# Performance work log

Measured on AMD Instinct MI355X. Metric: run time of the kernel, lower is better.

Reference implementation:

```python
import jax, jax.numpy as jnp
import numpy as np

NUM_BANDS = 8
WINDOW = 2048
OVERLAP = 1024
SR = 16000


def _band_mask(L):
    # Replicates torch: band = searchsorted(band_ranges, |freq|, left) - 1.
    # DC bin gives band=-1 which torch negative-indexes into the LAST band,
    # hence the mod. All bins satisfy band < NUM_BANDS, so all are assigned.
    freqs = np.fft.fftfreq(L, 1.0 / SR)
    ranges = np.linspace(0.0, SR / 2.0, NUM_BANDS + 1)
    idx = np.searchsorted(ranges, np.abs(freqs), side='left') - 1
    idx = idx % NUM_BANDS
    mask = (idx[None, :] == np.arange(NUM_BANDS)[:, None]).astype(np.float32)
    return jnp.asarray(mask)  # [bands, L]


def _band_signals(x):
    # mag*exp(i*phase) of masked bins == masked complex bins; ifft().real per band
    L = x.shape[-1]
    X = jnp.fft.fft(x)                         # [B, L] complex
    mask = _band_mask(L)                       # [bands, L]
    Xb = X[:, None, :] * mask[None, :, :]      # [B, bands, L]
    return jnp.fft.ifft(Xb).real               # [B, bands, L]


def _chunks(sig):
    L = sig.shape[-1]
    hop = WINDOW - OVERLAP
    n = (L - OVERLAP) // hop                   # num_chunks (static)
    idx = (jnp.arange(n) * hop)[:, None] + jnp.arange(WINDOW)[None, :]  # [n, W]
    return sig[:, :, idx]                       # [B, bands, n, W]


def _loudness(x):
    # BS.1770-style energy loudness (vectorized stand-in for the repo's
    # undefined `loudness` helper): -0.691 + 10*log10(mean square)
    ms = jnp.mean(x * x, axis=-1)
    return -0.691 + 10.0 * jnp.log10(ms + 1e-12)


def reference(watermarked_signals, original_signals):
    ro = _band_signals(original_signals)
    rw = _band_signals(watermarked_signals)
    lo = _loudness(_chunks(ro))                # [B, bands, n]
    lw = _loudness(_chunks(rw))
    lo = jnp.where(jnp.isnan(lo), 0.0, lo)
    lw = jnp.where(jnp.isnan(lw), 0.0, lw)
    diff = (lw - lo).reshape(-1)               # ordered (i, j, k) like the torch loop
    w = jax.nn.softmax(diff)
    return jnp.sum(w * diff)


def setup_inputs() -> dict:
    key = jax.random.key(0)
    k1, k2 = jax.random.split(key)
    B, L = 8, 160000
    return {
        'watermarked_signals': jax.random.normal(k1, (B, L), dtype=jnp.float32),
        'original_signals': jax.random.normal(k2, (B, L), dtype=jnp.float32),
    }
```

## Files before the change

### kernel.cpp

```cpp
#include <hip/hip_runtime.h>
#include <math.h>

constexpr int L      = 160000;
constexpr int BATCH  = 8;
constexpr int NB     = 8;
constexpr int NHOPS  = 156;
constexpr int NCHUNK = 155;
constexpr float TWO_PI = 6.28318530717958647692f;

__device__ __forceinline__ float2 cmulf(float2 a, float2 b) {
  return make_float2(a.x * b.x - a.y * b.y, a.x * b.y + a.y * b.x);
}

template <int SIGN>
__device__ __forceinline__ void bf4s(float2* v) {
  float2 t0 = make_float2(v[0].x + v[2].x, v[0].y + v[2].y);
  float2 t1 = make_float2(v[0].x - v[2].x, v[0].y - v[2].y);
  float2 t2 = make_float2(v[1].x + v[3].x, v[1].y + v[3].y);
  float2 t3 = make_float2(v[1].x - v[3].x, v[1].y - v[3].y);
  v[0] = make_float2(t0.x + t2.x, t0.y + t2.y);
  v[2] = make_float2(t0.x - t2.x, t0.y - t2.y);
  if constexpr (SIGN < 0) {
    v[1] = make_float2(t1.x + t3.y, t1.y - t3.x);
    v[3] = make_float2(t1.x - t3.y, t1.y + t3.x);
  } else {
    v[1] = make_float2(t1.x - t3.y, t1.y + t3.x);
    v[3] = make_float2(t1.x + t3.y, t1.y - t3.x);
  }
}

template <int SIGN>
__device__ __forceinline__ void bf5s(float2* v) {
  const float c1 = 0.30901699437494745f, s1 = 0.9510565162951535f;
  const float c2 = -0.8090169943749475f, s2 = 0.5877852522924731f;
  float2 t1 = make_float2(v[1].x + v[4].x, v[1].y + v[4].y);
  float2 t3 = make_float2(v[1].x - v[4].x, v[1].y - v[4].y);
  float2 t2 = make_float2(v[2].x + v[3].x, v[2].y + v[3].y);
  float2 t4 = make_float2(v[2].x - v[3].x, v[2].y - v[3].y);
  float2 a = make_float2(v[0].x + c1 * t1.x + c2 * t2.x, v[0].y + c1 * t1.y + c2 * t2.y);
  float2 b = make_float2(s1 * t3.x + s2 * t4.x, s1 * t3.y + s2 * t4.y);
  float2 c = make_float2(v[0].x + c2 * t1.x + c1 * t2.x, v[0].y + c2 * t1.y + c1 * t2.y);
  float2 d = make_float2(s2 * t3.x - s1 * t4.x, s2 * t3.y - s1 * t4.y);
  v[0] = make_float2(v[0].x + t1.x + t2.x, v[0].y + t1.y + t2.y);
  if constexpr (SIGN < 0) {
    v[1] = make_float2(a.x + b.y, a.y - b.x);
    v[4] = make_float2(a.x - b.y, a.y + b.x);
    v[2] = make_float2(c.x + d.y, c.y - d.x);
    v[3] = make_float2(c.x - d.y, c.y + d.x);
  } else {
    v[1] = make_float2(a.x - b.y, a.y + b.x);
    v[4] = make_float2(a.x + b.y, a.y - b.x);
    v[2] = make_float2(c.x - d.y, c.y + d.x);
    v[3] = make_float2(c.x + d.y, c.y - d.x);
  }
}

template <int R>
__device__ __forceinline__ void twapply(float2* v, float ang) {
#pragma unroll
  for (int r = 1; r < R; ++r) {
    float s, c;
    __sincosf(ang * (float)r, &s, &c);
    v[r] = cmulf(v[r], make_float2(c, s));
  }
}

__device__ __forceinline__ int rev3_5(int q) {
  int q5 = q / 5, q25 = q / 25;
  int d0 = q - 5 * q5, d1 = q5 - 5 * q25;
  return 25 * d0 + 5 * d1 + q25;
}

__device__ __forceinline__ int rev3_4(int q) {
  return ((q & 3) << 4) | (q & 12) | (q >> 4);
}

template <int SUB, int SIGN>
__device__ __forceinline__ void dif5_ip_stage(float2* a, int ln) {
  int i1 = ln, i2 = ln + 64;
  bool g2 = (i2 < 125);
  int j1 = i1 % SUB, j2 = i2 % SUB;
  int b1 = (i1 / SUB) * (5 * SUB) + j1;
  int b2 = (i2 / SUB) * (5 * SUB) + j2;
  float2 u[5], v[5];
#pragma unroll
  for (int r = 0; r < 5; ++r) u[r] = a[b1 + SUB * r];
  if (g2) {
#pragma unroll
    for (int r = 0; r < 5; ++r) v[r] = a[b2 + SUB * r];
  }
  bf5s<SIGN>(u);
  twapply<5>(u, (float)SIGN * (TWO_PI / (float)(5 * SUB)) * (float)j1);
  if (g2) {
    bf5s<SIGN>(v);
    twapply<5>(v, (float)SIGN * (TWO_PI / (float)(5 * SUB)) * (float)j2);
  }
#pragma unroll
  for (int r = 0; r < 5; ++r) a[b1 + SUB * r] = u[r];
  if (g2) {
#pragma unroll
    for (int r = 0; r < 5; ++r) a[b2 + SUB * r] = v[r];
  }
}

template <int SIGN>
__device__ __forceinline__ void dif625_ip(float2* a, int ln) {
  dif5_ip_stage<125, SIGN>(a, ln);
  dif5_ip_stage<25, SIGN>(a, ln);
  dif5_ip_stage<5, SIGN>(a, ln);
  int q1 = ln, q2 = ln + 64;
  bool g2 = (q2 < 125);
  float2 u[5], v[5];
#pragma unroll
  for (int r = 0; r < 5; ++r) u[r] = a[5 * q1 + r];
  if (g2) {
#pragma unroll
    for (int r = 0; r < 5; ++r) v[r] = a[5 * q2 + r];
  }
  bf5s<SIGN>(u);
  if (g2) bf5s<SIGN>(v);
  int rv1 = rev3_5(q1), rv2 = rev3_5(q2);
#pragma unroll
  for (int r = 0; r < 5; ++r) a[125 * r + rv1] = u[r];
  if (g2) {
#pragma unroll
    for (int r = 0; r < 5; ++r) a[125 * r + rv2] = v[r];
  }
}

template <int SIGN>
__device__ __forceinline__ void dif256_ip(float2* a, int ln) {
  {
    float2 u[4];
#pragma unroll
    for (int r = 0; r < 4; ++r) u[r] = a[ln + 64 * r];
    bf4s<SIGN>(u);
    twapply<4>(u, (float)SIGN * (TWO_PI / 256.0f) * (float)ln);
#pragma unroll
    for (int r = 0; r < 4; ++r) a[ln + 64 * r] = u[r];
  }
  {
    int j = ln & 15, b = 64 * (ln >> 4) + j;
    float2 u[4];
#pragma unroll
    for (int r = 0; r < 4; ++r) u[r] = a[b + 16 * r];
    bf4s<SIGN>(u);
    twapply<4>(u, (float)SIGN * (TWO_PI / 64.0f) * (float)j);
#pragma unroll
    for (int r = 0; r < 4; ++r) a[b + 16 * r] = u[r];
  }
  {
    int j = ln & 3, b = 16 * (ln >> 2) + j;
    float2 u[4];
#pragma unroll
    for (int r = 0; r < 4; ++r) u[r] = a[b + 4 * r];
    bf4s<SIGN>(u);
    twapply<4>(u, (float)SIGN * (TWO_PI / 16.0f) * (float)j);
#pragma unroll
    for (int r = 0; r < 4; ++r) a[b + 4 * r] = u[r];
  }
  {
    float2 u[4];
#pragma unroll
    for (int r = 0; r < 4; ++r) u[r] = a[4 * ln + r];
    bf4s<SIGN>(u);
    int rv = rev3_4(ln);
#pragma unroll
    for (int r = 0; r < 4; ++r) a[64 * r + rv] = u[r];
  }
}

__global__ __launch_bounds__(256) void f1_kernel(const float* __restrict__ win,
                                                 const float* __restrict__ oin,
                                                 float2* __restrict__ G) {
  __shared__ float2 A[4 * 625];
  int blk = blockIdx.x;
  int sig = blk >> 6, g = blk & 63;
  int n1base = g * 4;
  int tid = threadIdx.x;
  const float4* wp4 = (const float4*)(win + (size_t)sig * L);
  const float4* op4 = (const float4*)(oin + (size_t)sig * L);
  for (int r = tid; r < 625; r += 256) {
    float4 wv = wp4[r * 64 + g];
    float4 ov = op4[r * 64 + g];
    A[0 * 625 + r] = make_float2(wv.x, ov.x);
    A[1 * 625 + r] = make_float2(wv.y, ov.y);
    A[2 * 625 + r] = make_float2(wv.z, ov.z);
    A[3 * 625 + r] = make_float2(wv.w, ov.w);
  }
  __syncthreads();
  int wv_ = tid >> 6, ln = tid & 63;
  dif625_ip<-1>(A + wv_ * 625, ln);
  __syncthreads();
  for (int idx = tid; idx < 2500; idx += 256) {
    int k2 = idx >> 2, cc = idx & 3;
    int n1 = n1base + cc;
    float ang = -(TWO_PI / (float)L) * (float)(n1 * k2);
    float s, c;
    __sincosf(ang, &s, &c);
    G[(size_t)sig * L + k2 * 256 + n1] = cmulf(A[cc * 625 + k2], make_float2(c, s));
  }
}

__global__ __launch_bounds__(256) void f2_kernel(const float2* __restrict__ G,
                                                 float2* __restrict__ X) {
  __shared__ float2 A[4 * 257];
  int blk = blockIdx.x;
  int sig = blk / 157, gr = blk % 157;
  int k2base = gr * 4;
  int tid = threadIdx.x;
  int wv = tid >> 6, ln = tid & 63;
  int k2 = k2base + wv;
  float2* a = A + wv * 257;
  if (k2 < 625) {
#pragma unroll
    for (int r = 0; r < 4; ++r) a[ln + 64 * r] = G[(size_t)sig * L + k2 * 256 + ln + 64 * r];
    dif256_ip<-1>(a, ln);
  }
  __syncthreads();
  for (int idx = tid; idx < 1024; idx += 256) {
    int row = idx >> 8, k1 = idx & 255;
    int k2e = k2base + row;
    if (k2e < 625) X[(size_t)sig * L + k2e * 256 + k1] = A[row * 257 + k1];
  }
}

__global__ __launch_bounds__(256) void i1_kernel(const float2* __restrict__ X,
                                                 float2* __restrict__ H) {
  __shared__ float2 A[16 * 257];
  int blk = blockIdx.x;
  int gr = blk % 40, sb = blk / 40;
  int band = sb & 7, sig = sb >> 3;
  int k2base = gr * 16;
  int tid = threadIdx.x;
  int wv = tid >> 6, ln = tid & 63;
  int lo1, hi1, lo2, hi2;
  if (band < 7) {
    lo1 = 10000 * band + 1;        hi1 = 10000 * (band + 1);
    lo2 = L - 10000 * (band + 1);  hi2 = L - 10000 * band - 1;
  } else {
    lo1 = 70001; hi1 = 80000; lo2 = 80001; hi2 = 89999;
  }
  float2 zero = make_float2(0.0f, 0.0f);
#pragma unroll
  for (int i = 0; i < 4; ++i) {
    int lr = wv * 4 + i;
    int k2 = k2base + lr;
    float2* row = A + lr * 257;
    for (int k1 = ln; k1 < 256; k1 += 64) row[k1] = zero;
    if (k2 < 625) {
      const float2* Xr = X + (size_t)sig * L + k2 * 256;
      int s1 = (lo1 - k2 + 624) / 625;
      int e1 = (hi1 - k2) / 625; if (e1 > 255) e1 = 255;
      int s2 = (lo2 - k2 + 624) / 625;
      int e2 = (hi2 - k2) / 625; if (e2 > 255) e2 = 255;
      int c1 = e1 - s1 + 1;
      int c2 = e2 - s2 + 1;
      if (ln < c1) { int k1 = s1 + ln; row[k1] = Xr[k1]; }
      int l2 = ln - 32;
      if (l2 >= 0 && l2 < c2) { int k1 = s2 + l2; row[k1] = Xr[k1]; }
      if (band == 7 && k2 == 0 && ln == 0) row[0] = Xr[0];
      dif256_ip<1>(row, ln);
    }
  }
  __syncthreads();
  size_t obase = (size_t)(sig * NB + band) * L;
  int cc = tid & 15, n1o = tid >> 4;
  int k2e = k2base + cc;
  if (k2e < 625) {
    float a0 = (TWO_PI / (float)L) * (float)k2e;
    float s0, c0; __sincosf(a0 * (float)n1o, &s0, &c0);
    float ss, cs; __sincosf(a0 * 16.0f, &ss, &cs);
    float2 t = make_float2(c0, s0);
    float2 stp = make_float2(cs, ss);
#pragma unroll
    for (int it = 0; it < 16; ++it) {
      int n1 = n1o + 16 * it;
      H[obase + (size_t)n1 * 625 + k2e] = cmulf(A[cc * 257 + n1], t);
      t = cmulf(t, stp);
    }
  }
}

__global__ __launch_bounds__(256) void i2_kernel(const float2* __restrict__ H,
                                                 float* __restrict__ E) {
  __shared__ float2 A[4 * 625];
  __shared__ float P[4 * 2 * NHOPS];
  int blk = blockIdx.x;
  int g = blk & 31, sb = blk >> 5;
  int band = sb & 7, sig = sb >> 3;
  int tid = threadIdx.x;
  int wv = tid >> 6, ln = tid & 63;
  size_t base = (size_t)(sig * NB + band) * L;
  int n1A = 8 * g + wv, n1B = 8 * g + 4 + wv;
  const float2* HA = H + base + (size_t)n1A * 625;
  const float2* HB = H + base + (size_t)n1B * 625;
  int j1 = ln, j2 = ln + 64;
  bool g2 = (j2 < 125);
  float2 uA1[5], uA2[5], uB1[5], uB2[5];
#pragma unroll
  for (int r = 0; r < 5; ++r) uA1[r] = HA[j1 + 125 * r];
  if (g2) {
#pragma unroll
    for (int r = 0; r < 5; ++r) uA2[r] = HA[j2 + 125 * r];
  }
#pragma unroll
  for (int r = 0; r < 5; ++r) uB1[r] = HB[j1 + 125 * r];
  if (g2) {
#pragma unroll
    for (int r = 0; r < 5; ++r) uB2[r] = HB[j2 + 125 * r];
  }
  float2* a = A + wv * 625;
  float* Pw = P + wv * (2 * NHOPS);

  bf5s<1>(uA1);
  twapply<5>(uA1, (TWO_PI / 625.0f) * (float)j1);
#pragma unroll
  for (int r = 0; r < 5; ++r) a[j1 + 125 * r] = uA1[r];
  if (g2) {
    bf5s<1>(uA2);
    twapply<5>(uA2, (TWO_PI / 625.0f) * (float)j2);
#pragma unroll
    for (int r = 0; r < 5; ++r) a[j2 + 125 * r] = uA2[r];
  }
  dif5_ip_stage<25, 1>(a, ln);
  dif5_ip_stage<5, 1>(a, ln);
  {
    float2 u[5], v[5];
#pragma unroll
    for (int r = 0; r < 5; ++r) u[r] = a[5 * j1 + r];
    if (g2) {
#pragma unroll
      for (int r = 0; r < 5; ++r) v[r] = a[5 * j2 + r];
    }
    bf5s<1>(u);
    if (g2) bf5s<1>(v);
    int rv1 = rev3_5(j1), rv2 = rev3_5(j2);
#pragma unroll
    for (int r = 0; r < 5; ++r) a[125 * r + rv1] = u[r];
    if (g2) {
#pragma unroll
      for (int r = 0; r < 5; ++r) a[125 * r + rv2] = v[r];
    }
  }
  for (int h = ln; h < NHOPS; h += 64) {
    float ex = 0.0f, ey = 0.0f;
#pragma unroll
    for (int d = 0; d < 4; ++d) {
      float2 z = a[4 * h + d];
      ex += z.x * z.x;
      ey += z.y * z.y;
    }
    Pw[h] = ex;
    Pw[NHOPS + h] = ey;
  }

  bf5s<1>(uB1);
  twapply<5>(uB1, (TWO_PI / 625.0f) * (float)j1);
#pragma unroll
  for (int r = 0; r < 5; ++r) a[j1 + 125 * r] = uB1[r];
  if (g2) {
    bf5s<1>(uB2);
    twapply<5>(uB2, (TWO_PI / 625.0f) * (float)j2);
#pragma unroll
    for (int r = 0; r < 5; ++r) a[j2 + 125 * r] = uB2[r];
  }
  dif5_ip_stage<25, 1>(a, ln);
  dif5_ip_stage<5, 1>(a, ln);
  {
    float2 u[5], v[5];
#pragma unroll
    for (int r = 0; r < 5; ++r) u[r] = a[5 * j1 + r];
    if (g2) {
#pragma unroll
      for (int r = 0; r < 5; ++r) v[r] = a[5 * j2 + r];
    }
    bf5s<1>(u);
    if (g2) bf5s<1>(v);
    int rv1 = rev3_5(j1), rv2 = rev3_5(j2);
#pragma unroll
    for (int r = 0; r < 5; ++r) a[125 * r + rv1] = u[r];
    if (g2) {
#pragma unroll
      for (int r = 0; r < 5; ++r) a[125 * r + rv2] = v[r];
    }
  }
  for (int h = ln; h < NHOPS; h += 64) {
    float ex = 0.0f, ey = 0.0f;
#pragma unroll
    for (int d = 0; d < 4; ++d) {
      float2 z = a[4 * h + d];
      ex += z.x * z.x;
      ey += z.y * z.y;
    }
    Pw[h] += ex;
    Pw[NHOPS + h] += ey;
  }
  __syncthreads();
  int eb = (sig * NB + band) * NHOPS;
  for (int idx = tid; idx < 2 * NHOPS; idx += 256) {
    float v = P[idx] + P[2 * NHOPS + idx] + P[4 * NHOPS + idx] + P[6 * NHOPS + idx];
    int comp = idx / NHOPS, h = idx - comp * NHOPS;
    atomicAdd(&E[comp * (BATCH * NB * NHOPS) + eb + h], v);
  }
}

__global__ __launch_bounds__(1024) void finalize_kernel(const float* __restrict__ E,
                                                        float* __restrict__ out) {
  constexpr int ND = BATCH * NB * NCHUNK;
  constexpr float SC = (1.0f / 2048.0f) / ((float)L * (float)L);
  __shared__ float diffs[ND];
  __shared__ float sred[1024];
  int tid = threadIdx.x;
  for (int idx = tid; idx < ND; idx += 1024) {
    int sb = idx / NCHUNK;
    int k = idx - sb * NCHUNK;
    float msw = (E[sb * NHOPS + k] + E[sb * NHOPS + k + 1]) * SC;
    float mso = (E[64 * NHOPS + sb * NHOPS + k] + E[64 * NHOPS + sb * NHOPS + k + 1]) * SC;
    float lw = -0.691f + 10.0f * log10f(msw + 1e-12f);
    float lo = -0.691f + 10.0f * log10f(mso + 1e-12f);
    diffs[idx] = lw - lo;
  }
  __syncthreads();
  float mx = -3.4e38f;
  for (int idx = tid; idx < ND; idx += 1024) mx = fmaxf(mx, diffs[idx]);
  sred[tid] = mx;
  __syncthreads();
  for (int s = 512; s > 0; s >>= 1) {
    if (tid < s) sred[tid] = fmaxf(sred[tid], sred[tid + s]);
    __syncthreads();
  }
  float gmax = sred[0];
  __syncthreads();
  float se = 0.0f, swd = 0.0f;
  for (int idx = tid; idx < ND; idx += 1024) {
    float d = diffs[idx];
    float e = expf(d - gmax);
    se += e;
    swd += d * e;
  }
  sred[tid] = se; __syncthreads();
  for (int s = 512; s > 0; s >>= 1) { if (tid < s) sred[tid] += sred[tid + s]; __syncthreads(); }
  float tot = sred[0];
  __syncthreads();
  sred[tid] = swd; __syncthreads();
  for (int s = 512; s > 0; s >>= 1) { if (tid < s) sred[tid] += sred[tid + s]; __syncthreads(); }
  if (tid == 0) out[0] = sred[0] / tot;
}

extern "C" void kernel_launch(void* const* d_in, const int* in_sizes, int n_in,
                              void* d_out, int out_size, void* d_ws, size_t ws_size,
                              hipStream_t stream) {
  (void)in_sizes; (void)n_in; (void)out_size; (void)ws_size;
  char* ws = (char*)d_ws;
  float2* G = (float2*)ws;
  float2* X = (float2*)(ws + 10240000);
  float2* H = (float2*)(ws + 20480000);
  float*  E = (float*)(ws + 102400000);
  const float* w = (const float*)d_in[0];
  const float* o = (const float*)d_in[1];

  f1_kernel<<<dim3(BATCH * 64), dim3(256), 0, stream>>>(w, o, G);
  f2_kernel<<<dim3(BATCH * 157), dim3(256), 0, stream>>>(G, X);
  i1_kernel<<<dim3(BATCH * NB * 40), dim3(256), 0, stream>>>(X, H);
  hipMemsetAsync(E, 0, 2 * BATCH * NB * NHOPS * sizeof(float), stream);
  i2_kernel<<<dim3(BATCH * NB * 32), dim3(256), 0, stream>>>(H, E);
  finalize_kernel<<<dim3(1), dim3(1024), 0, stream>>>(E, (float*)d_out);
}
```

Baseline: 156.9 us.

## Use chained twiddles, widen i1 blocks to 1024 threads, fold memset into f1

Replaces per-radix sincos twiddle evaluation with one sincos per butterfly followed by complex-multiply chaining, in the i1 and i2 FFT stages. i1 now runs 1024 threads per block so each wave handles one 256-point row instead of four in sequence, and the transpose/twiddle output loop is reshaped to match. The workspace memset is moved into the f1 kernel to remove a separate launch. Chained twiddles trade transcendental work for multiplies at some cost in rounding accuracy, and the larger blocks change occupancy.

```diff
diff --git a/kernel.cpp b/kernel.cpp
--- a/kernel.cpp
+++ b/kernel.cpp
@@ -10,6 +10,12 @@
 
 __device__ __forceinline__ float2 cmulf(float2 a, float2 b) {
   return make_float2(a.x * b.x - a.y * b.y, a.x * b.y + a.y * b.x);
+}
+
+__device__ __forceinline__ float2 cisf(float a) {
+  float s, c;
+  __sincosf(a, &s, &c);
+  return make_float2(c, s);
 }
 
 template <int SIGN>
@@ -65,6 +71,14 @@
   }
 }
 
+template <int R>
+__device__ __forceinline__ void twchain(float2* v, float2 t1) {
+  float2 t = t1;
+  v[1] = cmulf(v[1], t);
+#pragma unroll
+  for (int r = 2; r < R; ++r) { t = cmulf(t, t1); v[r] = cmulf(v[r], t); }
+}
+
 __device__ __forceinline__ int rev3_5(int q) {
   int q5 = q / 5, q25 = q / 25;
   int d0 = q - 5 * q5, d1 = q5 - 5 * q25;
@@ -103,6 +117,34 @@
   }
 }
 
+template <int SUB>
+__device__ __forceinline__ void dif5_ip_stage_t(float2* a, int ln, float2 t1a, float2 t1b) {
+  int i1 = ln, i2 = ln + 64;
+  bool g2 = (i2 < 125);
+  int j1 = i1 % SUB, j2 = i2 % SUB;
+  int b1 = (i1 / SUB) * (5 * SUB) + j1;
+  int b2 = (i2 / SUB) * (5 * SUB) + j2;
+  float2 u[5], v[5];
+#pragma unroll
+  for (int r = 0; r < 5; ++r) u[r] = a[b1 + SUB * r];
+  if (g2) {
+#pragma unroll
+    for (int r = 0; r < 5; ++r) v[r] = a[b2 + SUB * r];
+  }
+  bf5s<1>(u);
+  twchain<5>(u, t1a);
+  if (g2) {
+    bf5s<1>(v);
+    twchain<5>(v, t1b);
+  }
+#pragma unroll
+  for (int r = 0; r < 5; ++r) a[b1 + SUB * r] = u[r];
+  if (g2) {
+#pragma unroll
+    for (int r = 0; r < 5; ++r) a[b2 + SUB * r] = v[r];
+  }
+}
+
 template <int SIGN>
 __device__ __forceinline__ void dif625_ip(float2* a, int ln) {
   dif5_ip_stage<125, SIGN>(a, ln);
@@ -170,11 +212,56 @@
   }
 }
 
+template <int SIGN>
+__device__ __forceinline__ void dif256c_ip(float2* a, int ln) {
+  {
+    float2 u[4];
+#pragma unroll
+    for (int r = 0; r < 4; ++r) u[r] = a[ln + 64 * r];
+    bf4s<SIGN>(u);
+    twchain<4>(u, cisf((float)SIGN * (TWO_PI / 256.0f) * (float)ln));
+#pragma unroll
+    for (int r = 0; r < 4; ++r) a[ln + 64 * r] = u[r];
+  }
+  {
+    int j = ln & 15, b = 64 * (ln >> 4) + j;
+    float2 u[4];
+#pragma unroll
+    for (int r = 0; r < 4; ++r) u[r] = a[b + 16 * r];
+    bf4s<SIGN>(u);
+    twchain<4>(u, cisf((float)SIGN * (TWO_PI / 64.0f) * (float)j));
+#pragma unroll
+    for (int r = 0; r < 4; ++r) a[b + 16 * r] = u[r];
+  }
+  {
+    int j = ln & 3, b = 16 * (ln >> 2) + j;
+    float2 u[4];
+#pragma unroll
+    for (int r = 0; r < 4; ++r) u[r] = a[b + 4 * r];
+    bf4s<SIGN>(u);
+    twchain<4>(u, cisf((float)SIGN * (TWO_PI / 16.0f) * (float)j));
+#pragma unroll
+    for (int r = 0; r < 4; ++r) a[b + 4 * r] = u[r];
+  }
+  {
+    float2 u[4];
+#pragma unroll
+    for (int r = 0; r < 4; ++r) u[r] = a[4 * ln + r];
+    bf4s<SIGN>(u);
+    int rv = rev3_4(ln);
+#pragma unroll
+    for (int r = 0; r < 4; ++r) a[64 * r + rv] = u[r];
+  }
+}
+
 __global__ __launch_bounds__(256) void f1_kernel(const float* __restrict__ win,
                                                  const float* __restrict__ oin,
-                                                 float2* __restrict__ G) {
+                                                 float2* __restrict__ G,
+                                                 float* __restrict__ E) {
   __shared__ float2 A[4 * 625];
   int blk = blockIdx.x;
+  int gid = blk * 256 + threadIdx.x;
+  if (gid < 2 * BATCH * NB * NHOPS) E[gid] = 0.0f;
   int sig = blk >> 6, g = blk & 63;
   int n1base = g * 4;
   int tid = threadIdx.x;
@@ -225,8 +312,8 @@
   }
 }
 
-__global__ __launch_bounds__(256) void i1_kernel(const float2* __restrict__ X,
-                                                 float2* __restrict__ H) {
+__global__ __launch_bounds__(1024) void i1_kernel(const float2* __restrict__ X,
+                                                  float2* __restrict__ H) {
   __shared__ float2 A[16 * 257];
   int blk = blockIdx.x;
   int gr = blk % 40, sb = blk / 40;
@@ -242,40 +329,34 @@
     lo1 = 70001; hi1 = 80000; lo2 = 80001; hi2 = 89999;
   }
   float2 zero = make_float2(0.0f, 0.0f);
-#pragma unroll
-  for (int i = 0; i < 4; ++i) {
-    int lr = wv * 4 + i;
-    int k2 = k2base + lr;
-    float2* row = A + lr * 257;
-    for (int k1 = ln; k1 < 256; k1 += 64) row[k1] = zero;
-    if (k2 < 625) {
-      const float2* Xr = X + (size_t)sig * L + k2 * 256;
-      int s1 = (lo1 - k2 + 624) / 625;
-      int e1 = (hi1 - k2) / 625; if (e1 > 255) e1 = 255;
-      int s2 = (lo2 - k2 + 624) / 625;
-      int e2 = (hi2 - k2) / 625; if (e2 > 255) e2 = 255;
-      int c1 = e1 - s1 + 1;
-      int c2 = e2 - s2 + 1;
-      if (ln < c1) { int k1 = s1 + ln; row[k1] = Xr[k1]; }
-      int l2 = ln - 32;
-      if (l2 >= 0 && l2 < c2) { int k1 = s2 + l2; row[k1] = Xr[k1]; }
-      if (band == 7 && k2 == 0 && ln == 0) row[0] = Xr[0];
-      dif256_ip<1>(row, ln);
-    }
+  int k2 = k2base + wv;
+  float2* row = A + wv * 257;
+  for (int k1 = ln; k1 < 256; k1 += 64) row[k1] = zero;
+  if (k2 < 625) {
+    const float2* Xr = X + (size_t)sig * L + k2 * 256;
+    int s1 = (lo1 - k2 + 624) / 625;
+    int e1 = (hi1 - k2) / 625; if (e1 > 255) e1 = 255;
+    int s2 = (lo2 - k2 + 624) / 625;
+    int e2 = (hi2 - k2) / 625; if (e2 > 255) e2 = 255;
+    int c1 = e1 - s1 + 1;
+    int c2 = e2 - s2 + 1;
+    if (ln < c1) { int k1 = s1 + ln; row[k1] = Xr[k1]; }
+    int l2 = ln - 32;
+    if (l2 >= 0 && l2 < c2) { int k1 = s2 + l2; row[k1] = Xr[k1]; }
+    if (band == 7 && k2 == 0 && ln == 0) row[0] = Xr[0];
+    dif256c_ip<1>(row, ln);
   }
   __syncthreads();
   size_t obase = (size_t)(sig * NB + band) * L;
-  int cc = tid & 15, n1o = tid >> 4;
+  int cc = tid & 15, n1g = tid >> 4;
   int k2e = k2base + cc;
   if (k2e < 625) {
     float a0 = (TWO_PI / (float)L) * (float)k2e;
-    float s0, c0; __sincosf(a0 * (float)n1o, &s0, &c0);
-    float ss, cs; __sincosf(a0 * 16.0f, &ss, &cs);
-    float2 t = make_float2(c0, s0);
-    float2 stp = make_float2(cs, ss);
-#pragma unroll
-    for (int it = 0; it < 16; ++it) {
-      int n1 = n1o + 16 * it;
+    float2 t = cisf(a0 * (float)n1g);
+    float2 stp = cisf(a0 * 64.0f);
+#pragma unroll
+    for (int it = 0; it < 4; ++it) {
+      int n1 = n1g + 64 * it;
       H[obase + (size_t)n1 * 625 + k2e] = cmulf(A[cc * 257 + n1], t);
       t = cmulf(t, stp);
     }
@@ -310,21 +391,27 @@
 #pragma unroll
     for (int r = 0; r < 5; ++r) uB2[r] = HB[j2 + 125 * r];
   }
+  float2 tS1a = cisf((TWO_PI / 625.0f) * (float)j1);
+  float2 tS1b = cisf((TWO_PI / 625.0f) * (float)j2);
+  float2 tS2a = cisf((TWO_PI / 125.0f) * (float)(j1 % 25));
+  float2 tS2b = cisf((TWO_PI / 125.0f) * (float)(j2 % 25));
+  float2 tS3a = cisf((TWO_PI / 25.0f) * (float)(j1 % 5));
+  float2 tS3b = cisf((TWO_PI / 25.0f) * (float)(j2 % 5));
   float2* a = A + wv * 625;
   float* Pw = P + wv * (2 * NHOPS);
 
   bf5s<1>(uA1);
-  twapply<5>(uA1, (TWO_PI / 625.0f) * (float)j1);
+  twchain<5>(uA1, tS1a);
 #pragma unroll
   for (int r = 0; r < 5; ++r) a[j1 + 125 * r] = uA1[r];
   if (g2) {
     bf5s<1>(uA2);
-    twapply<5>(uA2, (TWO_PI / 625.0f) * (float)j2);
+    twchain<5>(uA2, tS1b);
 #pragma unroll
     for (int r = 0; r < 5; ++r) a[j2 + 125 * r] = uA2[r];
   }
-  dif5_ip_stage<25, 1>(a, ln);
-  dif5_ip_stage<5, 1>(a, ln);
+  dif5_ip_stage_t<25>(a, ln, tS2a, tS2b);
+  dif5_ip_stage_t<5>(a, ln, tS3a, tS3b);
   {
     float2 u[5], v[5];
 #pragma unroll
@@ -356,17 +443,17 @@
   }
 
   bf5s<1>(uB1);
-  twapply<5>(uB1, (TWO_PI / 625.0f) * (float)j1);
+  twchain<5>(uB1, tS1a);
 #pragma unroll
   for (int r = 0; r < 5; ++r) a[j1 + 125 * r] = uB1[r];
   if (g2) {
     bf5s<1>(uB2);
-    twapply<5>(uB2, (TWO_PI / 625.0f) * (float)j2);
+    twchain<5>(uB2, tS1b);
 #pragma unroll
     for (int r = 0; r < 5; ++r) a[j2 + 125 * r] = uB2[r];
   }
-  dif5_ip_stage<25, 1>(a, ln);
-  dif5_ip_stage<5, 1>(a, ln);
+  dif5_ip_stage_t<25>(a, ln, tS2a, tS2b);
+  dif5_ip_stage_t<5>(a, ln, tS3a, tS3b);
   {
     float2 u[5], v[5];
 #pragma unroll
@@ -460,10 +547,9 @@
   const float* w = (const float*)d_in[0];
   const float* o = (const float*)d_in[1];
 
-  f1_kernel<<<dim3(BATCH * 64), dim3(256), 0, stream>>>(w, o, G);
+  f1_kernel<<<dim3(BATCH * 64), dim3(256), 0, stream>>>(w, o, G, E);
   f2_kernel<<<dim3(BATCH * 157), dim3(256), 0, stream>>>(G, X);
-  i1_kernel<<<dim3(BATCH * NB * 40), dim3(256), 0, stream>>>(X, H);
-  hipMemsetAsync(E, 0, 2 * BATCH * NB * NHOPS * sizeof(float), stream);
+  i1_kernel<<<dim3(BATCH * NB * 40), dim3(1024), 0, stream>>>(X, H);
   i2_kernel<<<dim3(BATCH * NB * 32), dim3(256), 0, stream>>>(H, E);
   finalize_kernel<<<dim3(1), dim3(1024), 0, stream>>>(E, (float*)d_out);
 }
```

Result: faster. 153.5 us (-2.1%).
